# Optimization experiments

Measured on AMD Instinct MI355X. Metric: run time of the kernel, lower is better.

Reference implementation:

```python
import jax, jax.numpy as jnp
import numpy as np

B, N, F_IN, F_OUT = 8, 2048, 64, 64
NEG_SLOPE = 0.01  # torch F.leaky_relu default


def setup_inputs() -> dict:
    key = jax.random.key(0)
    k_h, k_W, k_a = jax.random.split(key, 3)
    h = jax.random.normal(k_h, (B, N, F_IN), dtype=jnp.float32)
    adj = jnp.ones((B, N, N), dtype=jnp.float32)  # unused by the math, kept for signature fidelity
    # xavier_uniform init
    lim_W = float(np.sqrt(6.0 / (F_IN + F_OUT)))
    W = jax.random.uniform(k_W, (F_IN, F_OUT), minval=-lim_W, maxval=lim_W, dtype=jnp.float32)
    lim_a = float(np.sqrt(6.0 / (2 * F_OUT + 1)))
    a = jax.random.uniform(k_a, (2 * F_OUT, 1), minval=-lim_a, maxval=lim_a, dtype=jnp.float32)
    return {"h": h, "adj": adj, "W": W, "a": a}


def reference(h, adj, W, a):
    # Wh: [B, N, F_out]
    Wh = jnp.matmul(h, W)
    f_out = W.shape[1]
    # Exact decomposition of a^T [Wh_i || Wh_j] = a1.Wh_i + a2.Wh_j
    a1 = a[:f_out, 0]
    a2 = a[f_out:, 0]
    f1 = Wh @ a1  # [B, N] scores for source node i
    f2 = Wh @ a2  # [B, N] scores for target node j
    e = jax.nn.leaky_relu(f1[:, :, None] + f2[:, None, :], NEG_SLOPE)  # [B, N, N]
    attention = jax.nn.softmax(e, axis=-1)  # softmax over j (adj is NOT used, as in the source)
    h_prime = jnp.einsum('bij,bjf->bif', attention, Wh)
    return h_prime
```

## Files before the change

### kernel.cpp

```cpp
#include <hip/hip_runtime.h>
#include <math.h>

#define BB 8
#define NN 2048
#define FF 64
#define NBK 2048
#define RMIN (-16.0f)
#define BSCALE 64.0f


__global__ __launch_bounds__(256) void k1_gemm(const float* __restrict__ h,
                                               const float* __restrict__ W,
                                               const float* __restrict__ a,
                                               float* __restrict__ Wh,
                                               float* __restrict__ f1,
                                               float* __restrict__ f2,
                                               int* __restrict__ hist) {
  __shared__ float Wl[FF * FF];
  __shared__ float a1l[FF], a2l[FF];
  const int tid = threadIdx.x, lane = tid & 63, wv = tid >> 6;
  for (int i = tid; i < FF * FF; i += 256) Wl[i] = W[i];
  if (tid < FF) { a1l[tid] = a[tid]; a2l[tid] = a[FF + tid]; }
  __syncthreads();
  const int row0 = blockIdx.x * 16;
#pragma unroll
  for (int it = 0; it < 4; ++it) {
    const int row = row0 + it * 4 + wv;
    const float hreg = h[(size_t)row * FF + lane];
    float acc = 0.f;
#pragma unroll
    for (int k = 0; k < FF; ++k)
      acc = fmaf(__shfl(hreg, k, 64), Wl[k * FF + lane], acc);
    Wh[(size_t)row * FF + lane] = acc;
    float v1 = acc * a1l[lane], v2 = acc * a2l[lane];
#pragma unroll
    for (int o = 32; o > 0; o >>= 1) {
      v1 += __shfl_xor(v1, o, 64);
      v2 += __shfl_xor(v2, o, 64);
    }
    if (lane == 0) {
      f1[row] = v1; f2[row] = v2;
      int bk = (int)((v2 - RMIN) * BSCALE);
      bk = min(max(bk, 0), NBK - 1);
      atomicAdd(&hist[(row >> 11) * NBK + bk], 1);
    }
  }
}

__global__ __launch_bounds__(256) void k2_scan(const int* __restrict__ hist,
                                               int* __restrict__ startEx,
                                               int* __restrict__ cur) {
  __shared__ int wsum[4];
  const int b = blockIdx.x, tid = threadIdx.x;
  const int lane = tid & 63, wv = tid >> 6;
  int c[8]; int s = 0;
#pragma unroll
  for (int i = 0; i < 8; ++i) { c[i] = hist[b * NBK + tid * 8 + i]; s += c[i]; }
  int inc = s;
#pragma unroll
  for (int o = 1; o < 64; o <<= 1) {
    const int t = __shfl_up(inc, o, 64);
    if (lane >= o) inc += t;
  }
  if (lane == 63) wsum[wv] = inc;
  __syncthreads();
  int wbase = 0;
  for (int w = 0; w < wv; ++w) wbase += wsum[w];
  int run = wbase + inc - s;
#pragma unroll
  for (int i = 0; i < 8; ++i) {
    startEx[b * NBK + tid * 8 + i] = run;
    cur[b * NBK + tid * 8 + i] = run;
    run += c[i];
  }
}

__global__ __launch_bounds__(256) void k3_scatter(const float* __restrict__ f1,
                                                  const float* __restrict__ f2,
                                                  const int* __restrict__ startEx,
                                                  int* __restrict__ cur,
                                                  float* __restrict__ wlo,
                                                  float* __restrict__ whi,
                                                  int* __restrict__ sidx,
                                                  int* __restrict__ p0arr) {
  const int row = blockIdx.x * 256 + threadIdx.x;
  const int b = row >> 11;
  const float f2v = f2[row];
  int bk = (int)((f2v - RMIN) * BSCALE); bk = min(max(bk, 0), NBK - 1);
  const int pos = atomicAdd(&cur[b * NBK + bk], 1);
  wlo[b * NN + pos] = expf(0.01f * f2v);
  whi[b * NN + pos] = expf(f2v);
  sidx[b * NN + pos] = row & (NN - 1);
  const float t = -f1[row];
  int bq = (int)((t - RMIN) * BSCALE); bq = min(max(bq, 0), NBK - 1);
  p0arr[row] = startEx[b * NBK + bq];
}

__global__ __launch_bounds__(256) void k4_part(const float* __restrict__ Wh,
                                               const int* __restrict__ sidx,
                                               const float* __restrict__ wlo,
                                               const float* __restrict__ whi,
                                               double* __restrict__ part,
                                               double* __restrict__ zpart) {
  const int c = blockIdx.x, b = blockIdx.y, pass = blockIdx.z;
  const int tid = threadIdx.x, f = tid & 63, sub = tid >> 6;
  const int q0 = c * 128 + sub * 32;
  const int* __restrict__ sid = sidx + b * NN;
  const float* __restrict__ wv = (pass ? whi : wlo) + b * NN;
  const float* __restrict__ Whb = Wh + (size_t)b * NN * FF;
  double s = 0.0, sz = 0.0;
#pragma unroll 8
  for (int i = 0; i < 32; ++i) {
    const int q = q0 + i;
    const float w = wv[q];
    s += (double)w * (double)Whb[(size_t)sid[q] * FF + f];
    sz += (double)w;
  }
  const int k = c * 4 + sub;
  part[(((size_t)(pass * 8 + b)) * 64 + k) * 64 + f] = s;
  if (f == 0) zpart[(size_t)(pass * 8 + b) * 64 + k] = sz;
}

__global__ __launch_bounds__(256) void k5_sweep(const float* __restrict__ Wh,
                                                const int* __restrict__ sidx,
                                                const float* __restrict__ wlo,
                                                const float* __restrict__ whi,
                                                const double* __restrict__ part,
                                                const double* __restrict__ zpart,
                                                float* __restrict__ P_lo,
                                                float* __restrict__ S_hi,
                                                float* __restrict__ Pz,
                                                float* __restrict__ Sz) {
  const int c = blockIdx.x, b = blockIdx.y, pass = blockIdx.z;
  const int tid = threadIdx.x, f = tid & 63, sub = tid >> 6;
  const int q0 = c * 128 + sub * 32;
  const int k = c * 4 + sub;
  const double* __restrict__ Pp = part + ((size_t)(pass * 8 + b)) * 64 * 64;
  const double* __restrict__ Zp = zpart + (size_t)(pass * 8 + b) * 64;
  double run = 0.0, runz = 0.0;
  if (pass == 0) {
    for (int kk = 0; kk < k; ++kk) run += Pp[kk * 64 + f];
    if (f == 0) for (int kk = 0; kk < k; ++kk) runz += Zp[kk];
  } else {
    for (int kk = k + 1; kk < 64; ++kk) run += Pp[kk * 64 + f];
    if (f == 0) for (int kk = k + 1; kk < 64; ++kk) runz += Zp[kk];
  }
  const int* __restrict__ sid = sidx + b * NN;
  const float* __restrict__ wv = (pass ? whi : wlo) + b * NN;
  const float* __restrict__ Whb = Wh + (size_t)b * NN * FF;
  if (pass == 0) {
    float* __restrict__ P = P_lo + (size_t)b * (NN + 1) * FF;
    float* __restrict__ PzB = Pz + (size_t)b * (NN + 1);
#pragma unroll 8
    for (int i = 0; i < 32; ++i) {
      const int q = q0 + i;
      P[(size_t)q * FF + f] = (float)run;
      if (f == 0) PzB[q] = (float)runz;
      const float w = wv[q];
      run += (double)w * (double)Whb[(size_t)sid[q] * FF + f];
      runz += (double)w;
    }
    if (c == 15 && sub == 3) {
      P[(size_t)NN * FF + f] = (float)run;
      if (f == 0) PzB[NN] = (float)runz;
    }
  } else {
    float* __restrict__ S = S_hi + (size_t)b * (NN + 1) * FF;
    float* __restrict__ SzB = Sz + (size_t)b * (NN + 1);
#pragma unroll 8
    for (int i = 31; i >= 0; --i) {
      const int q = q0 + i;
      const float w = wv[q];
      run += (double)w * (double)Whb[(size_t)sid[q] * FF + f];
      runz += (double)w;
      S[(size_t)q * FF + f] = (float)run;
      if (f == 0) SzB[q] = (float)runz;
    }
    if (c == 15 && sub == 3) {
      S[(size_t)NN * FF + f] = 0.f;
      if (f == 0) SzB[NN] = 0.f;
    }
  }
}

__global__ __launch_bounds__(256) void k6_out(const float* __restrict__ f1,
                                              const int* __restrict__ p0arr,
                                              const float* __restrict__ S_hi,
                                              const float* __restrict__ P_lo,
                                              const float* __restrict__ Sz,
                                              const float* __restrict__ Pz,
                                              float* __restrict__ out) {
  const int tid = threadIdx.x, lane = tid & 63, wv = tid >> 6;
  const int row0 = blockIdx.x * 16;
#pragma unroll
  for (int it = 0; it < 4; ++it) {
    const int row = row0 + it * 4 + wv;
    const int b = row >> 11;
    const float f1v = f1[row];
    const int p0 = p0arr[row];
    const float w1 = expf(f1v), w2 = expf(0.01f * f1v);
    const size_t bp = (size_t)b * (NN + 1) + p0;
    const float num = w1 * S_hi[bp * FF + lane] + w2 * P_lo[bp * FF + lane];
    const float Z = w1 * Sz[bp] + w2 * Pz[bp];
    out[(size_t)row * FF + lane] = num / Z;
  }
}

extern "C" void kernel_launch(void* const* d_in, const int* in_sizes, int n_in,
                              void* d_out, int out_size, void* d_ws, size_t ws_size,
                              hipStream_t stream) {
  const float* h = (const float*)d_in[0];
  const float* W = (const float*)d_in[2];
  const float* a = (const float*)d_in[3];
  float* out = (float*)d_out;

  float* ws = (float*)d_ws;
  size_t o = 0;
  double* part  = (double*)(ws + o); o += (size_t)2 * BB * 64 * 64 * 2;
  double* zpart = (double*)(ws + o); o += (size_t)2 * BB * 64 * 2;
  float* Wh   = ws + o; o += (size_t)BB * NN * FF;
  float* f1   = ws + o; o += (size_t)BB * NN;
  float* f2   = ws + o; o += (size_t)BB * NN;
  float* wlo  = ws + o; o += (size_t)BB * NN;
  float* whi  = ws + o; o += (size_t)BB * NN;
  int* sidx   = (int*)(ws + o); o += (size_t)BB * NN;
  int* p0arr  = (int*)(ws + o); o += (size_t)BB * NN;
  int* hist   = (int*)(ws + o); o += (size_t)BB * NBK;
  int* cur    = (int*)(ws + o); o += (size_t)BB * NBK;
  int* startEx= (int*)(ws + o); o += (size_t)BB * NBK;
  float* P_lo = ws + o; o += (size_t)BB * (NN + 1) * FF;
  float* S_hi = ws + o; o += (size_t)BB * (NN + 1) * FF;
  float* Pz   = ws + o; o += (size_t)BB * (NN + 1);
  float* Sz   = ws + o; o += (size_t)BB * (NN + 1);

  hipMemsetAsync(hist, 0, (size_t)BB * NBK * sizeof(int), stream);
  k1_gemm<<<1024, 256, 0, stream>>>(h, W, a, Wh, f1, f2, hist);
  k2_scan<<<BB, 256, 0, stream>>>(hist, startEx, cur);
  k3_scatter<<<64, 256, 0, stream>>>(f1, f2, startEx, cur, wlo, whi, sidx, p0arr);
  dim3 g(16, BB, 2);
  k4_part<<<g, 256, 0, stream>>>(Wh, sidx, wlo, whi, part, zpart);
  k5_sweep<<<g, 256, 0, stream>>>(Wh, sidx, wlo, whi, part, zpart, P_lo, S_hi, Pz, Sz);
  k6_out<<<1024, 256, 0, stream>>>(f1, p0arr, S_hi, P_lo, Sz, Pz, out);
}
```

Measured before the change: 229.9 us.

## Replace counting sort and sweeps with atomic bucket accumulation and chunked prefix

Drops the histogram, scan, scatter and the two double-precision sweep kernels. The GEMM kernel now atomically accumulates exp-weighted Wh rows and weight sums straight into per-bucket arrays keyed by the f2 bucket. A small kernel then builds prefix and suffix bases over 16-bucket chunks, and the output kernel adds up to 16 buckets to finish each row's split. This removes several launches, the Wh round trip and the serial double-precision sweeps. In exchange it needs a larger memset, relies on contended float atomics whose summation order is nondeterministic, and does all accumulation in single precision.

```diff
diff --git a/kernel.cpp b/kernel.cpp
--- a/kernel.cpp
+++ b/kernel.cpp
@@ -5,17 +5,20 @@
 #define NN 2048
 #define FF 64
 #define NBK 2048
+#define CH 16
+#define NCH (NBK / CH)
 #define RMIN (-16.0f)
 #define BSCALE 64.0f
 
 
-__global__ __launch_bounds__(256) void k1_gemm(const float* __restrict__ h,
+__global__ __launch_bounds__(256) void ka_gemm(const float* __restrict__ h,
                                                const float* __restrict__ W,
                                                const float* __restrict__ a,
-                                               float* __restrict__ Wh,
                                                float* __restrict__ f1,
-                                               float* __restrict__ f2,
-                                               int* __restrict__ hist) {
+                                               float* __restrict__ Glo,
+                                               float* __restrict__ Ghi,
+                                               float* __restrict__ Gzlo,
+                                               float* __restrict__ Gzhi) {
   __shared__ float Wl[FF * FF];
   __shared__ float a1l[FF], a2l[FF];
   const int tid = threadIdx.x, lane = tid & 63, wv = tid >> 6;
@@ -31,164 +34,91 @@
 #pragma unroll
     for (int k = 0; k < FF; ++k)
       acc = fmaf(__shfl(hreg, k, 64), Wl[k * FF + lane], acc);
-    Wh[(size_t)row * FF + lane] = acc;
     float v1 = acc * a1l[lane], v2 = acc * a2l[lane];
 #pragma unroll
     for (int o = 32; o > 0; o >>= 1) {
       v1 += __shfl_xor(v1, o, 64);
       v2 += __shfl_xor(v2, o, 64);
     }
+    const int b = row >> 11;
+    int bk = (int)((v2 - RMIN) * BSCALE);
+    bk = min(max(bk, 0), NBK - 1);
+    const float wlo = expf(0.01f * v2), whi = expf(v2);
+    atomicAdd(&Glo[((size_t)(b * NBK + bk)) * FF + lane], wlo * acc);
+    atomicAdd(&Ghi[((size_t)(b * NBK + bk)) * FF + lane], whi * acc);
     if (lane == 0) {
-      f1[row] = v1; f2[row] = v2;
-      int bk = (int)((v2 - RMIN) * BSCALE);
-      bk = min(max(bk, 0), NBK - 1);
-      atomicAdd(&hist[(row >> 11) * NBK + bk], 1);
+      f1[row] = v1;
+      atomicAdd(&Gzlo[b * NBK + bk], wlo);
+      atomicAdd(&Gzhi[b * NBK + bk], whi);
     }
   }
 }
 
-__global__ __launch_bounds__(256) void k2_scan(const int* __restrict__ hist,
-                                               int* __restrict__ startEx,
-                                               int* __restrict__ cur) {
-  __shared__ int wsum[4];
-  const int b = blockIdx.x, tid = threadIdx.x;
-  const int lane = tid & 63, wv = tid >> 6;
-  int c[8]; int s = 0;
+__global__ __launch_bounds__(1024) void kb_base(const float* __restrict__ Glo,
+                                                const float* __restrict__ Ghi,
+                                                const float* __restrict__ Gzlo,
+                                                const float* __restrict__ Gzhi,
+                                                float* __restrict__ baseLo,
+                                                float* __restrict__ baseHi,
+                                                float* __restrict__ zbLo,
+                                                float* __restrict__ zbHi) {
+  __shared__ float part[NCH][FF];
+  __shared__ float zpart[NCH];
+  const int b = blockIdx.x >> 1, pass = blockIdx.x & 1;
+  const int t = threadIdx.x, f = t & 63, c = t >> 6;
+  const float* __restrict__ G = pass ? Ghi : Glo;
+  const float* __restrict__ Gz = pass ? Gzhi : Gzlo;
 #pragma unroll
-  for (int i = 0; i < 8; ++i) { c[i] = hist[b * NBK + tid * 8 + i]; s += c[i]; }
-  int inc = s;
+  for (int j = 0; j < 8; ++j) {
+    const int k = c * 8 + j;
+    const int u0 = k * CH;
+    float s = 0.f;
 #pragma unroll
-  for (int o = 1; o < 64; o <<= 1) {
-    const int t = __shfl_up(inc, o, 64);
-    if (lane >= o) inc += t;
+    for (int i = 0; i < CH; ++i)
+      s += G[((size_t)(b * NBK + u0 + i)) * FF + f];
+    part[k][f] = s;
+    if (f == 0) {
+      float z = 0.f;
+#pragma unroll
+      for (int i = 0; i < CH; ++i) z += Gz[b * NBK + u0 + i];
+      zpart[k] = z;
+    }
   }
-  if (lane == 63) wsum[wv] = inc;
   __syncthreads();
-  int wbase = 0;
-  for (int w = 0; w < wv; ++w) wbase += wsum[w];
-  int run = wbase + inc - s;
-#pragma unroll
-  for (int i = 0; i < 8; ++i) {
-    startEx[b * NBK + tid * 8 + i] = run;
-    cur[b * NBK + tid * 8 + i] = run;
-    run += c[i];
-  }
-}
-
-__global__ __launch_bounds__(256) void k3_scatter(const float* __restrict__ f1,
-                                                  const float* __restrict__ f2,
-                                                  const int* __restrict__ startEx,
-                                                  int* __restrict__ cur,
-                                                  float* __restrict__ wlo,
-                                                  float* __restrict__ whi,
-                                                  int* __restrict__ sidx,
-                                                  int* __restrict__ p0arr) {
-  const int row = blockIdx.x * 256 + threadIdx.x;
-  const int b = row >> 11;
-  const float f2v = f2[row];
-  int bk = (int)((f2v - RMIN) * BSCALE); bk = min(max(bk, 0), NBK - 1);
-  const int pos = atomicAdd(&cur[b * NBK + bk], 1);
-  wlo[b * NN + pos] = expf(0.01f * f2v);
-  whi[b * NN + pos] = expf(f2v);
-  sidx[b * NN + pos] = row & (NN - 1);
-  const float t = -f1[row];
-  int bq = (int)((t - RMIN) * BSCALE); bq = min(max(bq, 0), NBK - 1);
-  p0arr[row] = startEx[b * NBK + bq];
-}
-
-__global__ __launch_bounds__(256) void k4_part(const float* __restrict__ Wh,
-                                               const int* __restrict__ sidx,
-                                               const float* __restrict__ wlo,
-                                               const float* __restrict__ whi,
-                                               double* __restrict__ part,
-                                               double* __restrict__ zpart) {
-  const int c = blockIdx.x, b = blockIdx.y, pass = blockIdx.z;
-  const int tid = threadIdx.x, f = tid & 63, sub = tid >> 6;
-  const int q0 = c * 128 + sub * 32;
-  const int* __restrict__ sid = sidx + b * NN;
-  const float* __restrict__ wv = (pass ? whi : wlo) + b * NN;
-  const float* __restrict__ Whb = Wh + (size_t)b * NN * FF;
-  double s = 0.0, sz = 0.0;
-#pragma unroll 8
-  for (int i = 0; i < 32; ++i) {
-    const int q = q0 + i;
-    const float w = wv[q];
-    s += (double)w * (double)Whb[(size_t)sid[q] * FF + f];
-    sz += (double)w;
-  }
-  const int k = c * 4 + sub;
-  part[(((size_t)(pass * 8 + b)) * 64 + k) * 64 + f] = s;
-  if (f == 0) zpart[(size_t)(pass * 8 + b) * 64 + k] = sz;
-}
-
-__global__ __launch_bounds__(256) void k5_sweep(const float* __restrict__ Wh,
-                                                const int* __restrict__ sidx,
-                                                const float* __restrict__ wlo,
-                                                const float* __restrict__ whi,
-                                                const double* __restrict__ part,
-                                                const double* __restrict__ zpart,
-                                                float* __restrict__ P_lo,
-                                                float* __restrict__ S_hi,
-                                                float* __restrict__ Pz,
-                                                float* __restrict__ Sz) {
-  const int c = blockIdx.x, b = blockIdx.y, pass = blockIdx.z;
-  const int tid = threadIdx.x, f = tid & 63, sub = tid >> 6;
-  const int q0 = c * 128 + sub * 32;
-  const int k = c * 4 + sub;
-  const double* __restrict__ Pp = part + ((size_t)(pass * 8 + b)) * 64 * 64;
-  const double* __restrict__ Zp = zpart + (size_t)(pass * 8 + b) * 64;
-  double run = 0.0, runz = 0.0;
-  if (pass == 0) {
-    for (int kk = 0; kk < k; ++kk) run += Pp[kk * 64 + f];
-    if (f == 0) for (int kk = 0; kk < k; ++kk) runz += Zp[kk];
-  } else {
-    for (int kk = k + 1; kk < 64; ++kk) run += Pp[kk * 64 + f];
-    if (f == 0) for (int kk = k + 1; kk < 64; ++kk) runz += Zp[kk];
-  }
-  const int* __restrict__ sid = sidx + b * NN;
-  const float* __restrict__ wv = (pass ? whi : wlo) + b * NN;
-  const float* __restrict__ Whb = Wh + (size_t)b * NN * FF;
-  if (pass == 0) {
-    float* __restrict__ P = P_lo + (size_t)b * (NN + 1) * FF;
-    float* __restrict__ PzB = Pz + (size_t)b * (NN + 1);
-#pragma unroll 8
-    for (int i = 0; i < 32; ++i) {
-      const int q = q0 + i;
-      P[(size_t)q * FF + f] = (float)run;
-      if (f == 0) PzB[q] = (float)runz;
-      const float w = wv[q];
-      run += (double)w * (double)Whb[(size_t)sid[q] * FF + f];
-      runz += (double)w;
+  float* __restrict__ baseX = pass ? baseHi : baseLo;
+  float* __restrict__ zbX = pass ? zbHi : zbLo;
+  if (t < 64) {
+    float run = 0.f;
+    if (pass == 0) {
+      for (int k = 0; k < NCH; ++k) {
+        baseX[((size_t)(b * NCH + k)) * FF + f] = run;
+        run += part[k][f];
+      }
+    } else {
+      for (int k = NCH - 1; k >= 0; --k) {
+        baseX[((size_t)(b * NCH + k)) * FF + f] = run;
+        run += part[k][f];
+      }
     }
-    if (c == 15 && sub == 3) {
-      P[(size_t)NN * FF + f] = (float)run;
-      if (f == 0) PzB[NN] = (float)runz;
-    }
-  } else {
-    float* __restrict__ S = S_hi + (size_t)b * (NN + 1) * FF;
-    float* __restrict__ SzB = Sz + (size_t)b * (NN + 1);
-#pragma unroll 8
-    for (int i = 31; i >= 0; --i) {
-      const int q = q0 + i;
-      const float w = wv[q];
-      run += (double)w * (double)Whb[(size_t)sid[q] * FF + f];
-      runz += (double)w;
-      S[(size_t)q * FF + f] = (float)run;
-      if (f == 0) SzB[q] = (float)runz;
-    }
-    if (c == 15 && sub == 3) {
-      S[(size_t)NN * FF + f] = 0.f;
-      if (f == 0) SzB[NN] = 0.f;
+  } else if (t == 64) {
+    float run = 0.f;
+    if (pass == 0) {
+      for (int k = 0; k < NCH; ++k) { zbX[b * NCH + k] = run; run += zpart[k]; }
+    } else {
+      for (int k = NCH - 1; k >= 0; --k) { zbX[b * NCH + k] = run; run += zpart[k]; }
     }
   }
 }
 
-__global__ __launch_bounds__(256) void k6_out(const float* __restrict__ f1,
-                                              const int* __restrict__ p0arr,
-                                              const float* __restrict__ S_hi,
-                                              const float* __restrict__ P_lo,
-                                              const float* __restrict__ Sz,
-                                              const float* __restrict__ Pz,
+__global__ __launch_bounds__(256) void kc_out(const float* __restrict__ f1,
+                                              const float* __restrict__ Glo,
+                                              const float* __restrict__ Ghi,
+                                              const float* __restrict__ Gzlo,
+                                              const float* __restrict__ Gzhi,
+                                              const float* __restrict__ baseLo,
+                                              const float* __restrict__ baseHi,
+                                              const float* __restrict__ zbLo,
+                                              const float* __restrict__ zbHi,
                                               float* __restrict__ out) {
   const int tid = threadIdx.x, lane = tid & 63, wv = tid >> 6;
   const int row0 = blockIdx.x * 16;
@@ -197,12 +127,29 @@
     const int row = row0 + it * 4 + wv;
     const int b = row >> 11;
     const float f1v = f1[row];
-    const int p0 = p0arr[row];
+    const float thr = -f1v;
+    int bq = (int)((thr - RMIN) * BSCALE);
+    bq = min(max(bq, 0), NBK - 1);
+    const int k0 = bq >> 4;
+    const int u0 = k0 << 4;
+    float sHi = baseHi[((size_t)(b * NCH + k0)) * FF + lane];
+    float sLo = baseLo[((size_t)(b * NCH + k0)) * FF + lane];
+    float zHi = zbHi[b * NCH + k0];
+    float zLo = zbLo[b * NCH + k0];
+#pragma unroll
+    for (int i = 0; i < CH; ++i) {
+      const int u = u0 + i;
+      const size_t gi = ((size_t)(b * NBK + u)) * FF + lane;
+      if (u >= bq) {
+        sHi += Ghi[gi];
+        zHi += Gzhi[b * NBK + u];
+      } else {
+        sLo += Glo[gi];
+        zLo += Gzlo[b * NBK + u];
+      }
+    }
     const float w1 = expf(f1v), w2 = expf(0.01f * f1v);
-    const size_t bp = (size_t)b * (NN + 1) + p0;
-    const float num = w1 * S_hi[bp * FF + lane] + w2 * P_lo[bp * FF + lane];
-    const float Z = w1 * Sz[bp] + w2 * Pz[bp];
-    out[(size_t)row * FF + lane] = num / Z;
+    out[(size_t)row * FF + lane] = (w1 * sHi + w2 * sLo) / (w1 * zHi + w2 * zLo);
   }
 }
 
@@ -216,29 +163,19 @@
 
   float* ws = (float*)d_ws;
   size_t o = 0;
-  double* part  = (double*)(ws + o); o += (size_t)2 * BB * 64 * 64 * 2;
-  double* zpart = (double*)(ws + o); o += (size_t)2 * BB * 64 * 2;
-  float* Wh   = ws + o; o += (size_t)BB * NN * FF;
-  float* f1   = ws + o; o += (size_t)BB * NN;
-  float* f2   = ws + o; o += (size_t)BB * NN;
-  float* wlo  = ws + o; o += (size_t)BB * NN;
-  float* whi  = ws + o; o += (size_t)BB * NN;
-  int* sidx   = (int*)(ws + o); o += (size_t)BB * NN;
-  int* p0arr  = (int*)(ws + o); o += (size_t)BB * NN;
-  int* hist   = (int*)(ws + o); o += (size_t)BB * NBK;
-  int* cur    = (int*)(ws + o); o += (size_t)BB * NBK;
-  int* startEx= (int*)(ws + o); o += (size_t)BB * NBK;
-  float* P_lo = ws + o; o += (size_t)BB * (NN + 1) * FF;
-  float* S_hi = ws + o; o += (size_t)BB * (NN + 1) * FF;
-  float* Pz   = ws + o; o += (size_t)BB * (NN + 1);
-  float* Sz   = ws + o; o += (size_t)BB * (NN + 1);
+  float* Glo  = ws + o; o += (size_t)BB * NBK * FF;
+  float* Ghi  = ws + o; o += (size_t)BB * NBK * FF;
+  float* Gzlo = ws + o; o += (size_t)BB * NBK;
+  float* Gzhi = ws + o; o += (size_t)BB * NBK;
+  const size_t zero_bytes = o * sizeof(float);
+  float* f1     = ws + o; o += (size_t)BB * NN;
+  float* baseLo = ws + o; o += (size_t)BB * NCH * FF;
+  float* baseHi = ws + o; o += (size_t)BB * NCH * FF;
+  float* zbLo   = ws + o; o += (size_t)BB * NCH;
+  float* zbHi   = ws + o; o += (size_t)BB * NCH;
 
-  hipMemsetAsync(hist, 0, (size_t)BB * NBK * sizeof(int), stream);
-  k1_gemm<<<1024, 256, 0, stream>>>(h, W, a, Wh, f1, f2, hist);
-  k2_scan<<<BB, 256, 0, stream>>>(hist, startEx, cur);
-  k3_scatter<<<64, 256, 0, stream>>>(f1, f2, startEx, cur, wlo, whi, sidx, p0arr);
-  dim3 g(16, BB, 2);
-  k4_part<<<g, 256, 0, stream>>>(Wh, sidx, wlo, whi, part, zpart);
-  k5_sweep<<<g, 256, 0, stream>>>(Wh, sidx, wlo, whi, part, zpart, P_lo, S_hi, Pz, Sz);
-  k6_out<<<1024, 256, 0, stream>>>(f1, p0arr, S_hi, P_lo, Sz, Pz, out);
+  hipMemsetAsync(ws, 0, zero_bytes, stream);
+  ka_gemm<<<1024, 256, 0, stream>>>(h, W, a, f1, Glo, Ghi, Gzlo, Gzhi);
+  kb_base<<<16, 1024, 0, stream>>>(Glo, Ghi, Gzlo, Gzhi, baseLo, baseHi, zbLo, zbHi);
+  kc_out<<<1024, 256, 0, stream>>>(f1, Glo, Ghi, Gzlo, Gzhi, baseLo, baseHi, zbLo, zbHi, out);
 }
```

New measurement: 224.5 us. -2.4%, faster.
